# Kernel optimization log

Hardware: AMD Instinct MI355X
Metric: run time of the kernel (lower is better)

The kernel has to match this reference:

```python
import jax, jax.numpy as jnp
import numpy as np

B, N, D = 8, 128, 512

def setup_inputs() -> dict:
    key = jax.random.key(0)
    ks = jax.random.split(key, 8)
    def lin_w(k, fan_in, shape):
        bound = 1.0 / np.sqrt(fan_in)
        return jax.random.uniform(k, shape, jnp.float32, -bound, bound)
    return {
        "features": jax.random.normal(ks[0], (B, N, D), jnp.float32),
        "positions": jax.random.uniform(ks[1], (B, N, 2), jnp.float32),
        "W1": lin_w(ks[2], 2 * D + 2, (2 * D + 2, D)),
        "b1": lin_w(ks[3], 2 * D + 2, (D,)),
        "W2": lin_w(ks[4], D, (D, D // 2)),
        "b2": lin_w(ks[5], D, (D // 2,)),
        "W3": lin_w(ks[6], D // 2, (D // 2, 4)),
        "b3": lin_w(ks[7], D // 2, (4,)),
    }

def reference(features, positions, W1, b1, W2, b2, W3, b3):
    d = features.shape[-1]
    # Split first linear: concat([f1, f2, pos_diff]) @ W1 == f1@W1a + f2@W1b + pos_diff@W1c
    W1a, W1b, W1c = W1[:d], W1[d:2 * d], W1[2 * d:]
    h1 = jnp.einsum("bnd,dk->bnk", features, W1a)          # broadcast over axis 2 (j)
    h2 = jnp.einsum("bmd,dk->bmk", features, W1b)          # broadcast over axis 1 (i)
    pos_diff = positions[:, :, None, :] - positions[:, None, :, :]  # [B,N,N,2]
    h = h1[:, :, None, :] + h2[:, None, :, :] + jnp.einsum("bnmp,pk->bnmk", pos_diff, W1c) + b1
    h = jax.nn.relu(h)
    h = jax.nn.relu(jnp.einsum("bnmk,kl->bnml", h, W2) + b2)
    return jnp.einsum("bnml,lo->bnmo", h, W3) + b3          # [B,N,N,4]
```

## Files before the change

### kernel.cpp

```cpp
#include <hip/hip_runtime.h>
#include <hip/hip_bf16.h>

typedef unsigned short u16;
typedef unsigned int u32;
typedef __attribute__((ext_vector_type(8))) short bf16x8;
typedef __attribute__((ext_vector_type(4))) float floatx4;

__device__ __forceinline__ float bflo(u32 u){ union{u32 i; float f;}v; v.i=u<<16; return v.f; }
__device__ __forceinline__ float bfhi(u32 u){ union{u32 i; float f;}v; v.i=u&0xFFFF0000u; return v.f; }
__device__ __forceinline__ u16 f2bf(float f){
    union{float f;u32 i;}v; v.f=f; u32 r=v.i+0x7FFFu+((v.i>>16)&1u); return (u16)(r>>16);
}
__device__ __forceinline__ u32 pkbf(float a, float b){
    union { __hip_bfloat162 h; u32 u; } cv;
    cv.h = __float22bfloat162_rn(float2{a, b});
    return cv.u;
}

#define DD 512
#define NTOK 128

__global__ __launch_bounds__(256) void transpose_k(
    const float* __restrict__ W1, const float* __restrict__ W2,
    u16* __restrict__ W1aT, u16* __restrict__ W1bT, u16* __restrict__ W2T)
{
    const int z = blockIdx.z;
    const float* src; u16* dst; int rows, cols;
    if (z == 0)      { src = W1;             dst = W1aT; rows = 512; cols = 512; }
    else if (z == 1) { src = W1 + 512 * 512; dst = W1bT; rows = 512; cols = 512; }
    else             { src = W2;             dst = W2T;  rows = 512; cols = 256; }
    const int c0 = blockIdx.x * 32, r0 = blockIdx.y * 32;
    if (c0 >= cols || r0 >= rows) return;
    __shared__ u16 tile[32][33];
    const int tx = threadIdx.x & 31, ty = threadIdx.x >> 5;
#pragma unroll
    for (int i = 0; i < 4; ++i) {
        int r = ty + i * 8;
        tile[r][tx] = f2bf(src[(size_t)(r0 + r) * cols + (c0 + tx)]);
    }
    __syncthreads();
#pragma unroll
    for (int i = 0; i < 4; ++i) {
        int r = ty + i * 8;
        dst[(size_t)(c0 + r) * rows + (r0 + tx)] = tile[tx][r];
    }
}

__global__ __launch_bounds__(512) void gemm_layer1(
    const float* __restrict__ features, const u16* __restrict__ W1T,
    const float* __restrict__ b1, u16* __restrict__ Hf1b, u16* __restrict__ Hf2)
{
    const int bM = blockIdx.x, bN = blockIdx.y, z = blockIdx.z;
    const u16* Bt = W1T + (size_t)z * 512 * 512;
    u16* outp = z ? Hf2 : Hf1b;
    __shared__ __align__(16) u16 At[64 * 64];
    __shared__ __align__(16) u16 Btl[64 * 64];
    const int tid = threadIdx.x;
    const int wid = tid >> 6, lane = tid & 63, lrow = lane & 15, quad = lane >> 4;
    const int wm = wid >> 1, wn = wid & 1;

    floatx4 acc[2];
    acc[0] = (floatx4)(0.0f); acc[1] = (floatx4)(0.0f);

    const int m = tid >> 3, seg = tid & 7, sw = m & 7;
    for (int kc = 0; kc < 8; ++kc) {
        const int k0 = kc * 64;
        {
            const float4* src = (const float4*)(features + (size_t)(bM * 64 + m) * DD + k0 + seg * 8);
            float4 f0 = src[0], f1 = src[1];
            *(uint4*)(At + m * 64 + ((seg ^ sw) << 3)) =
                make_uint4(pkbf(f0.x, f0.y), pkbf(f0.z, f0.w), pkbf(f1.x, f1.y), pkbf(f1.z, f1.w));
        }
        {
            *(uint4*)(Btl + m * 64 + ((seg ^ sw) << 3)) =
                *(const uint4*)(Bt + (size_t)(bN * 64 + m) * DD + k0 + seg * 8);
        }
        __syncthreads();
#pragma unroll
        for (int ks = 0; ks < 2; ++ks) {
            const int ch = ks * 4 + quad;
            int r = wm * 16 + lrow;
            bf16x8 afr = *(const bf16x8*)(At + r * 64 + ((ch ^ (r & 7)) << 3));
#pragma unroll
            for (int j = 0; j < 2; ++j) {
                int c = wn * 32 + j * 16 + lrow;
                bf16x8 bfr = *(const bf16x8*)(Btl + c * 64 + ((ch ^ (c & 7)) << 3));
                acc[j] = __builtin_amdgcn_mfma_f32_16x16x32_bf16(afr, bfr, acc[j], 0, 0, 0);
            }
        }
        __syncthreads();
    }
#pragma unroll
    for (int j = 0; j < 2; ++j) {
        int col = bN * 64 + wn * 32 + j * 16 + lrow;
        float bb = z ? 0.0f : b1[col];
#pragma unroll
        for (int r = 0; r < 4; ++r) {
            int row = bM * 64 + wm * 16 + quad * 4 + r;
            outp[(size_t)row * DD + col] = f2bf(acc[j][r] + bb);
        }
    }
}

__global__ __launch_bounds__(512) void fused_main(
    const u16* __restrict__ Hf1b, const u16* __restrict__ Hf2,
    const u16* __restrict__ W2T, const float* __restrict__ W1,
    const float* __restrict__ b2, const float* __restrict__ W3,
    const float* __restrict__ b3, const float* __restrict__ positions,
    float* __restrict__ out)
{
    const int n = blockIdx.x, b = blockIdx.y;
    const int tid = threadIdx.x;
    const int base_bn = b * NTOK + n;
    const int wid = tid >> 6, lane = tid & 63, lrow = lane & 15, quad = lane >> 4;

    __shared__ __align__(16) u16 c0b[DD], c1b[DD], s1b[DD];
    __shared__ __align__(16) u16 w3t[16 * 264];
    __shared__ __align__(16) char mbuf[49152];
    u16* Atile = (u16*)mbuf;
    u16* Btile = (u16*)(mbuf + 16384);
    u16* gh    = (u16*)mbuf;

    {
        int k = tid;
        c0b[k] = f2bf(W1[(size_t)1024 * DD + k]);
        c1b[k] = f2bf(W1[(size_t)1025 * DD + k]);
        s1b[k] = Hf1b[(size_t)base_bn * DD + k];
    }
    {
        int c = tid & 15, kb = tid >> 4;
        int k0w = kb * 8;
        u32 wv[4];
#pragma unroll
        for (int p = 0; p < 4; ++p) {
            int ka = k0w + p * 2;
            u16 va = (c < 4) ? f2bf(W3[ka * 4 + c])       : (u16)0;
            u16 vb = (c < 4) ? f2bf(W3[(ka + 1) * 4 + c]) : (u16)0;
            wv[p] = (u32)va | ((u32)vb << 16);
        }
        *(uint2*)(w3t + c * 264 + k0w)     = make_uint2(wv[0], wv[1]);
        *(uint2*)(w3t + c * 264 + k0w + 4) = make_uint2(wv[2], wv[3]);
    }
    const int mrow = tid >> 2, seg = tid & 3, swA = mrow & 7;
    float px, py;
    {
        float pnx = positions[(size_t)base_bn * 2 + 0];
        float pny = positions[(size_t)base_bn * 2 + 1];
        px = pnx - positions[(size_t)(b * NTOK + mrow) * 2 + 0];
        py = pny - positions[(size_t)(b * NTOK + mrow) * 2 + 1];
    }
    __syncthreads();

    const int wm = wid >> 2, wn = wid & 3;
    floatx4 acc[4][4];
#pragma unroll
    for (int i = 0; i < 4; ++i)
#pragma unroll
        for (int j = 0; j < 4; ++j) acc[i][j] = (floatx4)(0.0f);

    const u16* hf2p = Hf2 + (size_t)(b * NTOK + mrow) * DD;

    for (int kc = 0; kc < 8; ++kc) {
        const int k0 = kc * 64;
        const int kb = k0 + seg * 16;
        {
            uint4 hv = *(const uint4*)(hf2p + kb);
            uint4 hw = *(const uint4*)(hf2p + kb + 8);
            uint4 sv = *(const uint4*)(s1b + kb);
            uint4 sw2 = *(const uint4*)(s1b + kb + 8);
            uint4 av = *(const uint4*)(c0b + kb);
            uint4 aw = *(const uint4*)(c0b + kb + 8);
            uint4 bv = *(const uint4*)(c1b + kb);
            uint4 bw = *(const uint4*)(c1b + kb + 8);
            auto hp = [&](u32 h, u32 s, u32 ca, u32 cb) -> u32 {
                float h0 = bflo(h) + bflo(s) + px * bflo(ca) + py * bflo(cb);
                float h1 = bfhi(h) + bfhi(s) + px * bfhi(ca) + py * bfhi(cb);
                return pkbf(fmaxf(h0, 0.0f), fmaxf(h1, 0.0f));
            };
            uint4 o0 = make_uint4(hp(hv.x, sv.x, av.x, bv.x), hp(hv.y, sv.y, av.y, bv.y),
                                  hp(hv.z, sv.z, av.z, bv.z), hp(hv.w, sv.w, av.w, bv.w));
            uint4 o1 = make_uint4(hp(hw.x, sw2.x, aw.x, bw.x), hp(hw.y, sw2.y, aw.y, bw.y),
                                  hp(hw.z, sw2.z, aw.z, bw.z), hp(hw.w, sw2.w, aw.w, bw.w));
            *(uint4*)(Atile + mrow * 64 + (((seg * 2    ) ^ swA) << 3)) = o0;
            *(uint4*)(Atile + mrow * 64 + (((seg * 2 + 1) ^ swA) << 3)) = o1;
        }
        {
            const int c = tid >> 1, sgB = tid & 1, swB = c & 7;
            const uint4* src = (const uint4*)(W2T + (size_t)c * DD + k0 + sgB * 32);
#pragma unroll
            for (int j = 0; j < 4; ++j)
                *(uint4*)(Btile + c * 64 + (((sgB * 4 + j) ^ swB) << 3)) = src[j];
        }
        __syncthreads();
#pragma unroll
        for (int ks = 0; ks < 2; ++ks) {
            const int ch = ks * 4 + quad;
            bf16x8 afr[4], bfr[4];
#pragma unroll
            for (int i = 0; i < 4; ++i) {
                int r = wm * 64 + i * 16 + lrow;
                afr[i] = *(const bf16x8*)(Atile + r * 64 + ((ch ^ (r & 7)) << 3));
            }
#pragma unroll
            for (int j = 0; j < 4; ++j) {
                int c = wn * 64 + j * 16 + lrow;
                bfr[j] = *(const bf16x8*)(Btile + c * 64 + ((ch ^ (c & 7)) << 3));
            }
#pragma unroll
            for (int i = 0; i < 4; ++i)
#pragma unroll
                for (int j = 0; j < 4; ++j)
                    acc[i][j] = __builtin_amdgcn_mfma_f32_16x16x32_bf16(afr[i], bfr[j], acc[i][j], 0, 0, 0);
        }
        __syncthreads();
    }

    float b2v[4];
#pragma unroll
    for (int j = 0; j < 4; ++j) b2v[j] = b2[wn * 64 + j * 16 + lrow];

    const int smrow = wid * 16;
    floatx4 acc3 = (floatx4)(0.0f);
#pragma unroll
    for (int half = 0; half < 2; ++half) {
        __syncthreads();
        if ((wn >> 1) == half) {
#pragma unroll
            for (int i = 0; i < 4; ++i)
#pragma unroll
                for (int j = 0; j < 4; ++j)
#pragma unroll
                    for (int r = 0; r < 4; ++r) {
                        int row = wm * 64 + i * 16 + quad * 4 + r;
                        int col = (wn & 1) * 64 + j * 16 + lrow;
                        gh[row * 136 + col] = f2bf(fmaxf(acc[i][j][r] + b2v[j], 0.0f));
                    }
        }
        __syncthreads();
#pragma unroll
        for (int ks = 0; ks < 4; ++ks) {
            bf16x8 gfrag = *(const bf16x8*)(gh + (smrow + lrow) * 136 + ks * 32 + quad * 8);
            bf16x8 wfrag = *(const bf16x8*)(w3t + lrow * 264 + half * 128 + ks * 32 + quad * 8);
            acc3 = __builtin_amdgcn_mfma_f32_16x16x32_bf16(gfrag, wfrag, acc3, 0, 0, 0);
        }
    }
    if (lrow < 4) {
        float bo = b3[lrow];
#pragma unroll
        for (int r = 0; r < 4; ++r) {
            int row = smrow + quad * 4 + r;
            out[(size_t)base_bn * 512 + row * 4 + lrow] = acc3[r] + bo;
        }
    }
}

extern "C" void kernel_launch(void* const* d_in, const int* in_sizes, int n_in,
                              void* d_out, int out_size, void* d_ws, size_t ws_size,
                              hipStream_t stream)
{
    const float* features  = (const float*)d_in[0];
    const float* positions = (const float*)d_in[1];
    const float* W1 = (const float*)d_in[2];
    const float* b1 = (const float*)d_in[3];
    const float* W2 = (const float*)d_in[4];
    const float* b2 = (const float*)d_in[5];
    const float* W3 = (const float*)d_in[6];
    const float* b3 = (const float*)d_in[7];
    float* out = (float*)d_out;

    char* ws = (char*)d_ws;
    u16* W1aT = (u16*)(ws);
    u16* W2T  = (u16*)(ws + 1048576);
    u16* Hf1b = (u16*)(ws + 1310720);
    u16* Hf2  = (u16*)(ws + 2359296);
    u16* W1bT = (u16*)(ws + 524288);

    transpose_k<<<dim3(16, 16, 3), 256, 0, stream>>>(W1, W2, W1aT, W1bT, W2T);
    gemm_layer1<<<dim3(16, 8, 2), 512, 0, stream>>>(features, W1aT, b1, Hf1b, Hf2);
    fused_main<<<dim3(128, 8), 512, 0, stream>>>(Hf1b, Hf2, W2T, W1, b2, W3, b3,
                                                 positions, out);
}
```

Before: 131.2 us.

## Fuse weight transpose into layer-1 GEMM, read W2 fragments directly from global

Drops the separate W1 transpose kernel. The layer-1 GEMM now reads W1 in fp32, converts it to bf16 and scatters it transposed into LDS, and the W2 transpose runs as an extra z-slice of the same launch, removing one kernel launch and a round trip through global memory. In the main fused kernel, the W2T tile is no longer staged through LDS; each wave loads its B fragments straight from global or L2. This shrinks shared memory and adds a launch bound hint aiming for more resident blocks, at the cost of uncoalesced, repeated global loads of W2 and scalar LDS scatter stores.

After: 157.6 us. 20.1% more time.

```diff
diff --git a/kernel.cpp b/kernel.cpp
--- a/kernel.cpp
+++ b/kernel.cpp
@@ -20,42 +20,36 @@
 #define DD 512
 #define NTOK 128
 
-__global__ __launch_bounds__(256) void transpose_k(
-    const float* __restrict__ W1, const float* __restrict__ W2,
-    u16* __restrict__ W1aT, u16* __restrict__ W1bT, u16* __restrict__ W2T)
+__global__ __launch_bounds__(512) void prep_k(
+    const float* __restrict__ features, const float* __restrict__ W1,
+    const float* __restrict__ W2, const float* __restrict__ b1,
+    u16* __restrict__ Hf1b, u16* __restrict__ Hf2, u16* __restrict__ W2T)
 {
     const int z = blockIdx.z;
-    const float* src; u16* dst; int rows, cols;
-    if (z == 0)      { src = W1;             dst = W1aT; rows = 512; cols = 512; }
-    else if (z == 1) { src = W1 + 512 * 512; dst = W1bT; rows = 512; cols = 512; }
-    else             { src = W2;             dst = W2T;  rows = 512; cols = 256; }
-    const int c0 = blockIdx.x * 32, r0 = blockIdx.y * 32;
-    if (c0 >= cols || r0 >= rows) return;
-    __shared__ u16 tile[32][33];
-    const int tx = threadIdx.x & 31, ty = threadIdx.x >> 5;
-#pragma unroll
-    for (int i = 0; i < 4; ++i) {
-        int r = ty + i * 8;
-        tile[r][tx] = f2bf(src[(size_t)(r0 + r) * cols + (c0 + tx)]);
-    }
-    __syncthreads();
-#pragma unroll
-    for (int i = 0; i < 4; ++i) {
-        int r = ty + i * 8;
-        dst[(size_t)(c0 + r) * rows + (r0 + tx)] = tile[tx][r];
-    }
-}
-
-__global__ __launch_bounds__(512) void gemm_layer1(
-    const float* __restrict__ features, const u16* __restrict__ W1T,
-    const float* __restrict__ b1, u16* __restrict__ Hf1b, u16* __restrict__ Hf2)
-{
-    const int bM = blockIdx.x, bN = blockIdx.y, z = blockIdx.z;
-    const u16* Bt = W1T + (size_t)z * 512 * 512;
+    const int tid = threadIdx.x;
+
+    if (z == 2) {
+        __shared__ u16 tile[32][33];
+        const int tx = tid & 31, ty = tid >> 5;
+        const int r0 = blockIdx.x * 32, c0 = blockIdx.y * 32;
+#pragma unroll
+        for (int i = 0; i < 2; ++i) {
+            int r = ty + i * 16;
+            tile[r][tx] = f2bf(W2[(size_t)(r0 + r) * 256 + (c0 + tx)]);
+        }
+        __syncthreads();
+#pragma unroll
+        for (int i = 0; i < 2; ++i) {
+            int c = ty + i * 16;
+            W2T[(size_t)(c0 + c) * 512 + (r0 + tx)] = tile[tx][c];
+        }
+        return;
+    }
+
+    const int bM = blockIdx.x, bN = blockIdx.y;
     u16* outp = z ? Hf2 : Hf1b;
     __shared__ __align__(16) u16 At[64 * 64];
     __shared__ __align__(16) u16 Btl[64 * 64];
-    const int tid = threadIdx.x;
     const int wid = tid >> 6, lane = tid & 63, lrow = lane & 15, quad = lane >> 4;
     const int wm = wid >> 1, wn = wid & 1;
 
@@ -63,6 +57,8 @@
     acc[0] = (floatx4)(0.0f); acc[1] = (floatx4)(0.0f);
 
     const int m = tid >> 3, seg = tid & 7, sw = m & 7;
+    const int kr = tid >> 3, csB = tid & 7;
+
     for (int kc = 0; kc < 8; ++kc) {
         const int k0 = kc * 64;
         {
@@ -72,8 +68,15 @@
                 make_uint4(pkbf(f0.x, f0.y), pkbf(f0.z, f0.w), pkbf(f1.x, f1.y), pkbf(f1.z, f1.w));
         }
         {
-            *(uint4*)(Btl + m * 64 + ((seg ^ sw) << 3)) =
-                *(const uint4*)(Bt + (size_t)(bN * 64 + m) * DD + k0 + seg * 8);
+            const float4* src = (const float4*)(W1 + (size_t)(z * 512 + k0 + kr) * DD + bN * 64 + csB * 8);
+            float4 g0 = src[0], g1 = src[1];
+            float f[8] = { g0.x, g0.y, g0.z, g0.w, g1.x, g1.y, g1.z, g1.w };
+            const int chunkB = (kr >> 3), offB = kr & 7;
+#pragma unroll
+            for (int i = 0; i < 8; ++i) {
+                int c = csB * 8 + i;
+                Btl[c * 64 + ((chunkB ^ i) << 3) + offB] = f2bf(f[i]);
+            }
         }
         __syncthreads();
 #pragma unroll
@@ -102,7 +105,7 @@
     }
 }
 
-__global__ __launch_bounds__(512) void fused_main(
+__global__ __launch_bounds__(512, 4) void fused_main(
     const u16* __restrict__ Hf1b, const u16* __restrict__ Hf2,
     const u16* __restrict__ W2T, const float* __restrict__ W1,
     const float* __restrict__ b2, const float* __restrict__ W3,
@@ -116,9 +119,8 @@
 
     __shared__ __align__(16) u16 c0b[DD], c1b[DD], s1b[DD];
     __shared__ __align__(16) u16 w3t[16 * 264];
-    __shared__ __align__(16) char mbuf[49152];
+    __shared__ __align__(16) char mbuf[34816];
     u16* Atile = (u16*)mbuf;
-    u16* Btile = (u16*)(mbuf + 16384);
     u16* gh    = (u16*)mbuf;
 
     {
@@ -128,8 +130,8 @@
         s1b[k] = Hf1b[(size_t)base_bn * DD + k];
     }
     {
-        int c = tid & 15, kb = tid >> 4;
-        int k0w = kb * 8;
+        int c = tid & 15, kb2 = tid >> 4;
+        int k0w = kb2 * 8;
         u32 wv[4];
 #pragma unroll
         for (int p = 0; p < 4; ++p) {
@@ -159,6 +161,7 @@
         for (int j = 0; j < 4; ++j) acc[i][j] = (floatx4)(0.0f);
 
     const u16* hf2p = Hf2 + (size_t)(b * NTOK + mrow) * DD;
+    const u16* w2p  = W2T + (size_t)(wn * 64 + lrow) * DD + quad * 8;
 
     for (int kc = 0; kc < 8; ++kc) {
         const int k0 = kc * 64;
@@ -184,27 +187,18 @@
             *(uint4*)(Atile + mrow * 64 + (((seg * 2    ) ^ swA) << 3)) = o0;
             *(uint4*)(Atile + mrow * 64 + (((seg * 2 + 1) ^ swA) << 3)) = o1;
         }
-        {
-            const int c = tid >> 1, sgB = tid & 1, swB = c & 7;
-            const uint4* src = (const uint4*)(W2T + (size_t)c * DD + k0 + sgB * 32);
-#pragma unroll
-            for (int j = 0; j < 4; ++j)
-                *(uint4*)(Btile + c * 64 + (((sgB * 4 + j) ^ swB) << 3)) = src[j];
-        }
         __syncthreads();
 #pragma unroll
         for (int ks = 0; ks < 2; ++ks) {
             const int ch = ks * 4 + quad;
             bf16x8 afr[4], bfr[4];
 #pragma unroll
+            for (int j = 0; j < 4; ++j)
+                bfr[j] = *(const bf16x8*)(w2p + (size_t)j * 16 * DD + k0 + ks * 32);
+#pragma unroll
             for (int i = 0; i < 4; ++i) {
                 int r = wm * 64 + i * 16 + lrow;
                 afr[i] = *(const bf16x8*)(Atile + r * 64 + ((ch ^ (r & 7)) << 3));
-            }
-#pragma unroll
-            for (int j = 0; j < 4; ++j) {
-                int c = wn * 64 + j * 16 + lrow;
-                bfr[j] = *(const bf16x8*)(Btile + c * 64 + ((ch ^ (c & 7)) << 3));
             }
 #pragma unroll
             for (int i = 0; i < 4; ++i)
@@ -269,14 +263,11 @@
     float* out = (float*)d_out;
 
     char* ws = (char*)d_ws;
-    u16* W1aT = (u16*)(ws);
-    u16* W2T  = (u16*)(ws + 1048576);
-    u16* Hf1b = (u16*)(ws + 1310720);
-    u16* Hf2  = (u16*)(ws + 2359296);
-    u16* W1bT = (u16*)(ws + 524288);
-
-    transpose_k<<<dim3(16, 16, 3), 256, 0, stream>>>(W1, W2, W1aT, W1bT, W2T);
-    gemm_layer1<<<dim3(16, 8, 2), 512, 0, stream>>>(features, W1aT, b1, Hf1b, Hf2);
+    u16* W2T  = (u16*)(ws);
+    u16* Hf1b = (u16*)(ws + 262144);
+    u16* Hf2  = (u16*)(ws + 1310720);
+
+    prep_k<<<dim3(16, 8, 3), 512, 0, stream>>>(features, W1, W2, b1, Hf1b, Hf2, W2T);
     fused_main<<<dim3(128, 8), 512, 0, stream>>>(Hf1b, Hf2, W2T, W1, b2, W3, b3,
                                                  positions, out);
 }
```
